# Kernel optimization log

Hardware: AMD Instinct MI355X
Metric: run time of the kernel (lower is better)

## Reference

```python
import jax, jax.numpy as jnp
import numpy as np

BINS = 50
MIN_V = 0.0
MAX_V = 1.0
SIGMA = 10.0
DELTA = (MAX_V - MIN_V) / BINS
EPS = 1e-8


def _soft_bin(v, centers):
    # v: [N, D] -> [N, bins, D]
    d = v[:, None, :] - centers[None, :, None]
    return jax.nn.sigmoid(SIGMA * (d + DELTA / 2)) - jax.nn.sigmoid(SIGMA * (d - DELTA / 2))


def setup_inputs() -> dict:
    key = jax.random.key(0)
    k1, k2 = jax.random.split(key)
    im1 = jax.random.uniform(k1, (8, 384, 384), dtype=jnp.float32)
    im2 = jax.random.uniform(k2, (8, 384, 384), dtype=jnp.float32)
    return {"im1": im1, "im2": im2}


def reference(im1, im2):
    n = im1.shape[0]
    x = im1.reshape(n, -1)
    y = im2.reshape(n, -1)
    centers = MIN_V + DELTA * (jnp.arange(BINS, dtype=jnp.float32) + 0.5)
    xs = _soft_bin(x, centers)  # [N, bins, D]
    ys = _soft_bin(y, centers)  # [N, bins, D]
    hgram = jnp.einsum('nbd,ncd->nbc', xs, ys)  # [N, bins, bins]
    # NOTE: original normalizes by the sum over the WHOLE batch
    p_xy = hgram / jnp.sum(hgram)
    marginal_x = jnp.sum(p_xy, axis=2)  # [N, bins]
    marginal_y = jnp.sum(p_xy, axis=1)  # [N, bins]
    joined = marginal_x[:, :, None] * marginal_y[:, None, :]  # [N, bins, bins]
    mi_per = jnp.sum(
        p_xy * (jnp.log(p_xy + EPS) - jnp.log(joined + EPS)), axis=(1, 2)
    )
    return jnp.sum(mi_per)  # reduction='sum'
```

## Files before the change

### kernel.cpp

```cpp
#include <hip/hip_runtime.h>


#define D_TOTAL   147456
#define NBATCH    8
#define BINS      50
#define NEDGE     28
#define KSLICES   96
#define KC        256
#define SLICE_LEN (D_TOTAL / KSLICES)
#define ITERS     (SLICE_LEN / KC)
#define LDS_STR   280

typedef _Float16 half8  __attribute__((ext_vector_type(8)));
typedef __fp16   fp16x2 __attribute__((ext_vector_type(2)));
typedef float    f32x4  __attribute__((ext_vector_type(4)));

struct Tab { float c[NEDGE]; };
constexpr Tab make_tab() {
    Tab t{};
    double c = 0.6703200460356393;
    const double lam = 1.4918246976412703;
    for (int i = 0; i < NEDGE; ++i) { t.c[i] = (float)c; c *= lam; }
    return t;
}
constexpr Tab TAB = make_tab();

__global__ __launch_bounds__(256, 3) void hgram_kernel(const float* __restrict__ im1,
                                                       const float* __restrict__ im2,
                                                       float* __restrict__ hg) {
    __shared__ __align__(16) _Float16 Xs[32][LDS_STR];
    __shared__ __align__(16) _Float16 Ys[32][LDS_STR];

    const int tid   = threadIdx.x;
    const int slice = blockIdx.x;
    const int n     = blockIdx.y;
    const int base  = n * D_TOTAL + slice * SLICE_LEN;

    {
        unsigned* px = (unsigned*)&Xs[28][0];
        unsigned* py = (unsigned*)&Ys[28][0];
        for (int i = tid; i < 4 * LDS_STR / 2; i += 256) { px[i] = 0u; py[i] = 0u; }
    }

    const int h    = tid & 127;
    const int isY  = tid >> 7;
    const float2* src2 = (const float2*)((isY ? im2 : im1) + base);
    _Float16* plane = isY ? &Ys[0][0] : &Xs[0][0];
    _Float16* dst   = plane + 2 * h;

    const int lane = tid & 63;
    const int w    = tid >> 6;
    const int r0   = (w & 1) << 4;
    const int c0   = (w >> 1) << 4;
    const int frow = lane & 15;
    const int kg   = (lane >> 4) << 3;

    f32x4 acc = {0.f, 0.f, 0.f, 0.f};

    float2 v = src2[h];
    for (int it = 0; it < ITERS; ++it) {
        float2 nv = {0.f, 0.f};
        if (it + 1 < ITERS) nv = src2[(it + 1) * (KC / 2) + h];
        {
            const float Ea = __builtin_amdgcn_exp2f(v.x * -14.426950408889634f);
            const float Eb = __builtin_amdgcn_exp2f(v.y * -14.426950408889634f);
            #pragma unroll
            for (int i = 0; i < NEDGE; ++i) {
                const float c = TAB.c[i];
                float ta = __builtin_amdgcn_rcpf(__builtin_fmaf(c * Ea, 0.00390625f, 0.00390625f));
                float tb = __builtin_amdgcn_rcpf(__builtin_fmaf(c * Eb, 0.00390625f, 0.00390625f));
                fp16x2 p = __builtin_amdgcn_cvt_pkrtz(ta, tb);
                *(fp16x2*)(dst + i * LDS_STR) = p;
            }
        }
        __syncthreads();
        #pragma unroll
        for (int ks = 0; ks < 8; ++ks) {
            const int k0 = ks * 32 + kg;
            half8 a = *(const half8*)&Xs[r0 + frow][k0];
            half8 b = *(const half8*)&Ys[c0 + frow][k0];
            acc = __builtin_amdgcn_mfma_f32_16x16x32_f16(a, b, acc, 0, 0, 0);
        }
        __syncthreads();
        v = nv;
    }

    float* hgn = hg + n * 1024;
    const int gj = c0 + (lane & 15);
    const int ri = r0 + ((lane >> 4) << 2);
    if (gj < NEDGE) {
        #pragma unroll
        for (int r = 0; r < 4; ++r) {
            const int gi = ri + r;
            if (gi < NEDGE) atomicAdd(&hgn[gi * 32 + gj], acc[r]);
        }
    }
}

__global__ __launch_bounds__(1024) void finalize_kernel(const float* __restrict__ hg,
                                                        float* __restrict__ out) {
    __shared__ float Gs[NBATCH][NEDGE][29];
    __shared__ float mx[NBATCH][BINS], my[NBATCH][BINS];
    __shared__ float red[16];
    __shared__ float sT;
    const int tid = threadIdx.x;

    for (int idx = tid; idx < NBATCH * NEDGE * NEDGE; idx += 1024) {
        int n = idx / (NEDGE * NEDGE);
        int rem = idx - n * (NEDGE * NEDGE);
        int r = rem / NEDGE, c = rem - r * NEDGE;
        Gs[n][r][c] = hg[n * 1024 + r * 32 + c];
    }
    __syncthreads();

    if (tid < 2 * NBATCH * BINS) {
        const int which = (tid >= NBATCH * BINS) ? 1 : 0;
        const int t2 = which ? tid - NBATCH * BINS : tid;
        const int n = t2 / BINS, b = t2 - n * BINS;
        const int q = b >> 1;
        float w0, w1, w2, w3;
        if (b & 1) { w0 = -1.f; w1 = 9.f; w2 = -7.f; w3 = -1.f; }
        else       { w0 =  1.f; w1 = 7.f; w2 = -9.f; w3 =  1.f; }
        float m;
        if (which == 0) {
            m = w0 * (Gs[n][q][1]   - Gs[n][q][26])
              + w1 * (Gs[n][q+1][1] - Gs[n][q+1][26])
              + w2 * (Gs[n][q+2][1] - Gs[n][q+2][26])
              + w3 * (Gs[n][q+3][1] - Gs[n][q+3][26]);
            mx[n][b] = m * 0.0625f;
        } else {
            m = w0 * (Gs[n][1][q]   - Gs[n][26][q])
              + w1 * (Gs[n][1][q+1] - Gs[n][26][q+1])
              + w2 * (Gs[n][1][q+2] - Gs[n][26][q+2])
              + w3 * (Gs[n][1][q+3] - Gs[n][26][q+3]);
            my[n][b] = m * 0.0625f;
        }
    }
    if (tid == 0) {
        float t = 0.f;
        for (int n = 0; n < NBATCH; ++n)
            t += Gs[n][1][1] - Gs[n][1][26] - Gs[n][26][1] + Gs[n][26][26];
        sT = t;
    }
    __syncthreads();

    const float invT = 1.0f / sT;
    const float invT2 = invT * invT;
    float mi = 0.f;
    for (int task = tid; task < NBATCH * 25 * 25; task += 1024) {
        const int n = task / 625;
        const int rem = task - n * 625;
        const int bp = rem / 25, cp = rem - bp * 25;
        float g[4][4];
        #pragma unroll
        for (int r = 0; r < 4; ++r)
            #pragma unroll
            for (int s = 0; s < 4; ++s) g[r][s] = Gs[n][bp + r][cp + s];
        float rde[4], rdo[4];
        #pragma unroll
        for (int r = 0; r < 4; ++r) {
            rde[r] =  g[r][0] + 7.f * g[r][1] - 9.f * g[r][2] + g[r][3];
            rdo[r] = -g[r][0] + 9.f * g[r][1] - 7.f * g[r][2] - g[r][3];
        }
        const float hee = ( rde[0] + 7.f*rde[1] - 9.f*rde[2] + rde[3]) * (1.f/256.f);
        const float heo = ( rdo[0] + 7.f*rdo[1] - 9.f*rdo[2] + rdo[3]) * (1.f/256.f);
        const float hoe = (-rde[0] + 9.f*rde[1] - 7.f*rde[2] - rde[3]) * (1.f/256.f);
        const float hoo = (-rdo[0] + 9.f*rdo[1] - 7.f*rdo[2] - rdo[3]) * (1.f/256.f);
        const int b0 = 2 * bp, c0 = 2 * cp;
        {
            float p = hee * invT, jo = mx[n][b0] * my[n][c0] * invT2;
            mi += p * (__logf(p + 1e-8f) - __logf(jo + 1e-8f));
        }
        {
            float p = heo * invT, jo = mx[n][b0] * my[n][c0 + 1] * invT2;
            mi += p * (__logf(p + 1e-8f) - __logf(jo + 1e-8f));
        }
        {
            float p = hoe * invT, jo = mx[n][b0 + 1] * my[n][c0] * invT2;
            mi += p * (__logf(p + 1e-8f) - __logf(jo + 1e-8f));
        }
        {
            float p = hoo * invT, jo = mx[n][b0 + 1] * my[n][c0 + 1] * invT2;
            mi += p * (__logf(p + 1e-8f) - __logf(jo + 1e-8f));
        }
    }
    #pragma unroll
    for (int o = 32; o > 0; o >>= 1) mi += __shfl_down(mi, o, 64);
    if ((tid & 63) == 0) red[tid >> 6] = mi;
    __syncthreads();
    if (tid == 0) {
        float t = 0.f;
        for (int i = 0; i < 16; ++i) t += red[i];
        out[0] = t;
    }
}

extern "C" void kernel_launch(void* const* d_in, const int* in_sizes, int n_in,
                              void* d_out, int out_size, void* d_ws, size_t ws_size,
                              hipStream_t stream) {
    const float* im1 = (const float*)d_in[0];
    const float* im2 = (const float*)d_in[1];
    float* out = (float*)d_out;
    float* hg  = (float*)d_ws;

    (void)hipMemsetAsync(d_ws, 0, NBATCH * 1024 * sizeof(float), stream);
    hgram_kernel<<<dim3(KSLICES, NBATCH), dim3(256), 0, stream>>>(im1, im2, hg);
    finalize_kernel<<<dim3(1), dim3(1024), 0, stream>>>(hg, out);
}
```

Baseline: 83.07 us.

## Fuse memset, histogram and finalize into one cooperative kernel

```diff
diff --git a/kernel.cpp b/kernel.cpp
--- a/kernel.cpp
+++ b/kernel.cpp
@@ -1,4 +1,5 @@
 #include <hip/hip_runtime.h>
+#include <hip/hip_cooperative_groups.h>
 
 
 #define D_TOTAL   147456
@@ -10,6 +11,7 @@
 #define SLICE_LEN (D_TOTAL / KSLICES)
 #define ITERS     (SLICE_LEN / KC)
 #define LDS_STR   280
+#define NBLOCKS   (KSLICES * NBATCH)
 
 typedef _Float16 half8  __attribute__((ext_vector_type(8)));
 typedef __fp16   fp16x2 __attribute__((ext_vector_type(2)));
@@ -25,27 +27,36 @@
 }
 constexpr Tab TAB = make_tab();
 
-__global__ __launch_bounds__(256, 3) void hgram_kernel(const float* __restrict__ im1,
-                                                       const float* __restrict__ im2,
-                                                       float* __restrict__ hg) {
-    __shared__ __align__(16) _Float16 Xs[32][LDS_STR];
-    __shared__ __align__(16) _Float16 Ys[32][LDS_STR];
+__global__ __launch_bounds__(256, 3) void mi_fused(const float* __restrict__ im1,
+                                                   const float* __restrict__ im2,
+                                                   float* __restrict__ hg,
+                                                   float* __restrict__ out) {
+    __shared__ __align__(16) _Float16 SH[2][32][LDS_STR];
 
     const int tid   = threadIdx.x;
     const int slice = blockIdx.x;
     const int n     = blockIdx.y;
     const int base  = n * D_TOTAL + slice * SLICE_LEN;
+    unsigned* const done = (unsigned*)(hg + NBATCH * 1024);
+
+    if (slice == 0) {
+        float* z = hg + n * 1024;
+        for (int i = tid; i < 1024; i += 256)
+            __hip_atomic_store(&z[i], 0.0f, __ATOMIC_RELAXED, __HIP_MEMORY_SCOPE_AGENT);
+        if (n == 0 && tid == 0)
+            __hip_atomic_store(done, 0u, __ATOMIC_RELAXED, __HIP_MEMORY_SCOPE_AGENT);
+    }
 
     {
-        unsigned* px = (unsigned*)&Xs[28][0];
-        unsigned* py = (unsigned*)&Ys[28][0];
+        unsigned* px = (unsigned*)&SH[0][28][0];
+        unsigned* py = (unsigned*)&SH[1][28][0];
         for (int i = tid; i < 4 * LDS_STR / 2; i += 256) { px[i] = 0u; py[i] = 0u; }
     }
 
     const int h    = tid & 127;
     const int isY  = tid >> 7;
     const float2* src2 = (const float2*)((isY ? im2 : im1) + base);
-    _Float16* plane = isY ? &Ys[0][0] : &Xs[0][0];
+    _Float16* plane = &SH[isY][0][0];
     _Float16* dst   = plane + 2 * h;
 
     const int lane = tid & 63;
@@ -77,13 +88,16 @@
         #pragma unroll
         for (int ks = 0; ks < 8; ++ks) {
             const int k0 = ks * 32 + kg;
-            half8 a = *(const half8*)&Xs[r0 + frow][k0];
-            half8 b = *(const half8*)&Ys[c0 + frow][k0];
+            half8 a = *(const half8*)&SH[0][r0 + frow][k0];
+            half8 b = *(const half8*)&SH[1][c0 + frow][k0];
             acc = __builtin_amdgcn_mfma_f32_16x16x32_f16(a, b, acc, 0, 0, 0);
         }
         __syncthreads();
         v = nv;
     }
+
+    __threadfence();
+    cooperative_groups::this_grid().sync();
 
     float* hgn = hg + n * 1024;
     const int gj = c0 + (lane & 15);
@@ -95,67 +109,75 @@
             if (gi < NEDGE) atomicAdd(&hgn[gi * 32 + gj], acc[r]);
         }
     }
-}
-
-__global__ __launch_bounds__(1024) void finalize_kernel(const float* __restrict__ hg,
-                                                        float* __restrict__ out) {
-    __shared__ float Gs[NBATCH][NEDGE][29];
-    __shared__ float mx[NBATCH][BINS], my[NBATCH][BINS];
-    __shared__ float red[16];
-    __shared__ float sT;
-    const int tid = threadIdx.x;
-
-    for (int idx = tid; idx < NBATCH * NEDGE * NEDGE; idx += 1024) {
-        int n = idx / (NEDGE * NEDGE);
-        int rem = idx - n * (NEDGE * NEDGE);
-        int r = rem / NEDGE, c = rem - r * NEDGE;
-        Gs[n][r][c] = hg[n * 1024 + r * 32 + c];
-    }
-    __syncthreads();
-
-    if (tid < 2 * NBATCH * BINS) {
-        const int which = (tid >= NBATCH * BINS) ? 1 : 0;
-        const int t2 = which ? tid - NBATCH * BINS : tid;
-        const int n = t2 / BINS, b = t2 - n * BINS;
-        const int q = b >> 1;
+
+    __syncthreads();
+    if (tid == 0)
+        __hip_atomic_fetch_add(done, 1u, __ATOMIC_RELEASE, __HIP_MEMORY_SCOPE_AGENT);
+    if (slice != 0 || n != 0) return;
+
+    if (tid == 0) {
+        while (__hip_atomic_load(done, __ATOMIC_ACQUIRE, __HIP_MEMORY_SCOPE_AGENT) < (unsigned)NBLOCKS)
+            __builtin_amdgcn_s_sleep(8);
+    }
+    __syncthreads();
+
+    float* const F  = (float*)&SH[0][0][0];
+    float* const MX = F + 6496;
+    float* const MY = F + 6896;
+    #define GS(nn,rr,cc) F[((nn)*NEDGE+(rr))*29+(cc)]
+
+    for (int idx = tid; idx < NBATCH * NEDGE * NEDGE; idx += 256) {
+        int b   = idx / (NEDGE * NEDGE);
+        int rem = idx - b * (NEDGE * NEDGE);
+        int r = rem / NEDGE, c2 = rem - r * NEDGE;
+        GS(b, r, c2) = __hip_atomic_load(&hg[b * 1024 + r * 32 + c2],
+                                         __ATOMIC_RELAXED, __HIP_MEMORY_SCOPE_AGENT);
+    }
+    __syncthreads();
+
+    for (int t = tid; t < 2 * NBATCH * BINS; t += 256) {
+        const int which = (t >= NBATCH * BINS) ? 1 : 0;
+        const int t2 = which ? t - NBATCH * BINS : t;
+        const int b = t2 / BINS, bb = t2 - b * BINS;
+        const int q = bb >> 1;
         float w0, w1, w2, w3;
-        if (b & 1) { w0 = -1.f; w1 = 9.f; w2 = -7.f; w3 = -1.f; }
-        else       { w0 =  1.f; w1 = 7.f; w2 = -9.f; w3 =  1.f; }
+        if (bb & 1) { w0 = -1.f; w1 = 9.f; w2 = -7.f; w3 = -1.f; }
+        else        { w0 =  1.f; w1 = 7.f; w2 = -9.f; w3 =  1.f; }
         float m;
         if (which == 0) {
-            m = w0 * (Gs[n][q][1]   - Gs[n][q][26])
-              + w1 * (Gs[n][q+1][1] - Gs[n][q+1][26])
-              + w2 * (Gs[n][q+2][1] - Gs[n][q+2][26])
-              + w3 * (Gs[n][q+3][1] - Gs[n][q+3][26]);
-            mx[n][b] = m * 0.0625f;
+            m = w0 * (GS(b,q,1)   - GS(b,q,26))
+              + w1 * (GS(b,q+1,1) - GS(b,q+1,26))
+              + w2 * (GS(b,q+2,1) - GS(b,q+2,26))
+              + w3 * (GS(b,q+3,1) - GS(b,q+3,26));
+            MX[b * BINS + bb] = m * 0.0625f;
         } else {
-            m = w0 * (Gs[n][1][q]   - Gs[n][26][q])
-              + w1 * (Gs[n][1][q+1] - Gs[n][26][q+1])
-              + w2 * (Gs[n][1][q+2] - Gs[n][26][q+2])
-              + w3 * (Gs[n][1][q+3] - Gs[n][26][q+3]);
-            my[n][b] = m * 0.0625f;
+            m = w0 * (GS(b,1,q)   - GS(b,26,q))
+              + w1 * (GS(b,1,q+1) - GS(b,26,q+1))
+              + w2 * (GS(b,1,q+2) - GS(b,26,q+2))
+              + w3 * (GS(b,1,q+3) - GS(b,26,q+3));
+            MY[b * BINS + bb] = m * 0.0625f;
         }
     }
     if (tid == 0) {
         float t = 0.f;
-        for (int n = 0; n < NBATCH; ++n)
-            t += Gs[n][1][1] - Gs[n][1][26] - Gs[n][26][1] + Gs[n][26][26];
-        sT = t;
-    }
-    __syncthreads();
-
-    const float invT = 1.0f / sT;
+        for (int b = 0; b < NBATCH; ++b)
+            t += GS(b,1,1) - GS(b,1,26) - GS(b,26,1) + GS(b,26,26);
+        F[7300] = t;
+    }
+    __syncthreads();
+
+    const float invT = 1.0f / F[7300];
     const float invT2 = invT * invT;
     float mi = 0.f;
-    for (int task = tid; task < NBATCH * 25 * 25; task += 1024) {
-        const int n = task / 625;
-        const int rem = task - n * 625;
+    for (int task = tid; task < NBATCH * 25 * 25; task += 256) {
+        const int b   = task / 625;
+        const int rem = task - b * 625;
         const int bp = rem / 25, cp = rem - bp * 25;
         float g[4][4];
         #pragma unroll
         for (int r = 0; r < 4; ++r)
             #pragma unroll
-            for (int s = 0; s < 4; ++s) g[r][s] = Gs[n][bp + r][cp + s];
+            for (int s = 0; s < 4; ++s) g[r][s] = GS(b, bp + r, cp + s);
         float rde[4], rdo[4];
         #pragma unroll
         for (int r = 0; r < 4; ++r) {
@@ -166,33 +188,29 @@
         const float heo = ( rdo[0] + 7.f*rdo[1] - 9.f*rdo[2] + rdo[3]) * (1.f/256.f);
         const float hoe = (-rde[0] + 9.f*rde[1] - 7.f*rde[2] - rde[3]) * (1.f/256.f);
         const float hoo = (-rdo[0] + 9.f*rdo[1] - 7.f*rdo[2] - rdo[3]) * (1.f/256.f);
-        const int b0 = 2 * bp, c0 = 2 * cp;
-        {
-            float p = hee * invT, jo = mx[n][b0] * my[n][c0] * invT2;
-            mi += p * (__logf(p + 1e-8f) - __logf(jo + 1e-8f));
-        }
-        {
-            float p = heo * invT, jo = mx[n][b0] * my[n][c0 + 1] * invT2;
-            mi += p * (__logf(p + 1e-8f) - __logf(jo + 1e-8f));
-        }
-        {
-            float p = hoe * invT, jo = mx[n][b0 + 1] * my[n][c0] * invT2;
-            mi += p * (__logf(p + 1e-8f) - __logf(jo + 1e-8f));
-        }
-        {
-            float p = hoo * invT, jo = mx[n][b0 + 1] * my[n][c0 + 1] * invT2;
+        const int b0 = 2 * bp, c0f = 2 * cp;
+        {
+            float p = hee * invT, jo = MX[b * BINS + b0] * MY[b * BINS + c0f] * invT2;
+            mi += p * (__logf(p + 1e-8f) - __logf(jo + 1e-8f));
+        }
+        {
+            float p = heo * invT, jo = MX[b * BINS + b0] * MY[b * BINS + c0f + 1] * invT2;
+            mi += p * (__logf(p + 1e-8f) - __logf(jo + 1e-8f));
+        }
+        {
+            float p = hoe * invT, jo = MX[b * BINS + b0 + 1] * MY[b * BINS + c0f] * invT2;
+            mi += p * (__logf(p + 1e-8f) - __logf(jo + 1e-8f));
+        }
+        {
+            float p = hoo * invT, jo = MX[b * BINS + b0 + 1] * MY[b * BINS + c0f + 1] * invT2;
             mi += p * (__logf(p + 1e-8f) - __logf(jo + 1e-8f));
         }
     }
     #pragma unroll
     for (int o = 32; o > 0; o >>= 1) mi += __shfl_down(mi, o, 64);
-    if ((tid & 63) == 0) red[tid >> 6] = mi;
-    __syncthreads();
-    if (tid == 0) {
-        float t = 0.f;
-        for (int i = 0; i < 16; ++i) t += red[i];
-        out[0] = t;
-    }
+    if ((tid & 63) == 0) F[7296 + (tid >> 6)] = mi;
+    __syncthreads();
+    if (tid == 0) out[0] = F[7296] + F[7297] + F[7298] + F[7299];
 }
 
 extern "C" void kernel_launch(void* const* d_in, const int* in_sizes, int n_in,
@@ -203,7 +221,8 @@
     float* out = (float*)d_out;
     float* hg  = (float*)d_ws;
 
-    (void)hipMemsetAsync(d_ws, 0, NBATCH * 1024 * sizeof(float), stream);
-    hgram_kernel<<<dim3(KSLICES, NBATCH), dim3(256), 0, stream>>>(im1, im2, hg);
-    finalize_kernel<<<dim3(1), dim3(1024), 0, stream>>>(hg, out);
+    void* args[4] = { (void*)&im1, (void*)&im2, (void*)&hg, (void*)&out };
+    (void)hipLaunchCooperativeKernel((const void*)mi_fused,
+                                     dim3(KSLICES, NBATCH), dim3(256),
+                                     args, 0, stream);
 }
```

Measured after the change: 244.5 us. +194.3%, slower.
